# Performance work log

Hardware: AMD Instinct MI355X
Metric: run time of the kernel (lower is better)

## Reference

```python
import jax, jax.numpy as jnp
import numpy as np

T, B, I, H = 256, 32, 128, 256
CLIP = 2.0

def setup_inputs() -> dict:
    key = jax.random.key(0)
    ks = jax.random.split(key, 10)
    si, sh = 1.0 / np.sqrt(I), 1.0 / np.sqrt(H)
    return {
        "x":     jax.random.normal(ks[0], (T, B, I), jnp.float32),
        "Wx":    jax.random.normal(ks[1], (4 * H, I), jnp.float32) * si,
        "bx":    jax.random.normal(ks[2], (4 * H,), jnp.float32) * si,
        "Wh":    jax.random.normal(ks[3], (4 * H, H), jnp.float32) * sh,
        "bh":    jax.random.normal(ks[4], (4 * H,), jnp.float32) * sh,
        "w_mod": jax.random.normal(ks[5], (1, H), jnp.float32) * sh,
        "b_mod": jax.random.normal(ks[6], (1,), jnp.float32) * sh,
        "w_fan": jax.random.normal(ks[7], (H, 1), jnp.float32),
        "b_fan": jax.random.normal(ks[8], (H,), jnp.float32),
        "alpha": 1e-4 * jax.random.uniform(ks[9], (H, H), jnp.float32),
    }

def reference(x, Wx, bx, Wh, bh, w_mod, b_mod, w_fan, b_fan, alpha):
    Bn = x.shape[1]
    # precompute input projection for all timesteps: [T, B, 4H]
    xf = jnp.einsum('tbi,gi->tbg', x, Wx) + bx

    def step(state, xf_t):
        h, c, hebb = state  # h,c: [B,H]; hebb: [B,H,H]
        fioj = xf_t + h @ Wh.T + bh                     # [B,4H]
        f = jax.nn.sigmoid(fioj[:, :H])
        i = jax.nn.sigmoid(fioj[:, H:2 * H])
        o = jax.nn.sigmoid(fioj[:, 2 * H:3 * H])
        # h_pred @ (alpha * hebb) : batched vec-mat product
        plast = jnp.einsum('bh,hk,bhk->bk', h, alpha, hebb)
        j = jnp.tanh(fioj[:, 3 * H:] + plast)
        c_new = f * c + i * j
        h_new = o * jnp.tanh(c_new)
        eta = jnp.tanh(c_new @ w_mod.T + b_mod)          # [B,1]
        myeta = eta * w_fan[:, 0] + b_fan                # [B,H] (Linear(1,H) fanout)
        # delta_hebb = outer(h_pred, j); eta modulates along the j axis
        hebb_new = jnp.clip(hebb + myeta[:, None, :] * (h[:, :, None] * j[:, None, :]),
                            -CLIP, CLIP)
        return (h_new, c_new, hebb_new), h_new

    init = (jnp.zeros((Bn, H), jnp.float32),
            jnp.zeros((Bn, H), jnp.float32),
            jnp.zeros((Bn, H, H), jnp.float32))
    (h, c, hebb), hs = jax.lax.scan(step, init, xf)
    return hs, h, c, hebb
```

## Files before the change

kernel.cpp:

```cpp
#include <hip/hip_runtime.h>


#define TT 256
#define BB 32
#define II 128
#define HH 256
#define G4 1024

typedef _Float16 h2_t __attribute__((ext_vector_type(2)));
typedef unsigned long long u64;

__device__ __forceinline__ float sigm(float x) {
    return 1.0f / (1.0f + __expf(-x));
}
__device__ __forceinline__ float tanhfast(float x) {
    return 1.0f - 2.0f / (__expf(2.0f * x) + 1.0f);
}
__device__ __forceinline__ unsigned pkh(float lo, float hi) {
    h2_t v;
    v.x = (_Float16)lo;
    v.y = (_Float16)hi;
    return __builtin_bit_cast(unsigned, v);
}

#if __has_builtin(__builtin_amdgcn_fdot2)
__device__ __forceinline__ float dot2(unsigned a, unsigned b, float c) {
    return __builtin_amdgcn_fdot2(__builtin_bit_cast(h2_t, a),
                                  __builtin_bit_cast(h2_t, b), c, false);
}
#else
__device__ __forceinline__ float dot2(unsigned a, unsigned b, float c) {
    h2_t av = __builtin_bit_cast(h2_t, a), bv = __builtin_bit_cast(h2_t, b);
    return c + (float)av.x * (float)bv.x + (float)av.y * (float)bv.y;
}
#endif

__device__ __forceinline__ h2_t pkfma(h2_t a, h2_t b, h2_t c) {
#if __has_builtin(__builtin_elementwise_fma)
    return __builtin_elementwise_fma(a, b, c);
#else
    return a * b + c;
#endif
}
__device__ __forceinline__ h2_t clip2h(h2_t x) {
    const h2_t lo = {(_Float16)-2.0f, (_Float16)-2.0f};
    const h2_t hi = {(_Float16)2.0f, (_Float16)2.0f};
#if __has_builtin(__builtin_elementwise_max) && __has_builtin(__builtin_elementwise_min)
    return __builtin_elementwise_min(__builtin_elementwise_max(x, lo), hi);
#else
    h2_t r = x;
    r.x = r.x < lo.x ? lo.x : (r.x > hi.x ? hi.x : r.x);
    r.y = r.y < lo.y ? lo.y : (r.y > hi.y ? hi.y : r.y);
    return r;
#endif
}

__device__ __forceinline__ u64 spin_slot(const u64* fp, const u64* dp,
                                         unsigned tag) {
    u64 v;
    int it = 0;
    for (;;) {
        if ((it & 3) == 3) {
            v = __hip_atomic_load(dp, __ATOMIC_RELAXED,
                                  __HIP_MEMORY_SCOPE_AGENT);
        } else {
            asm volatile("global_load_dwordx2 %0, %1, off sc0\n\t"
                         "s_waitcnt vmcnt(0)"
                         : "=v"(v) : "v"(fp));
        }
        ++it;
        if ((unsigned)(v >> 32) == tag) return v;
    }
}

__global__ __launch_bounds__(256) void prep_wdx(const float* __restrict__ Wh,
                                                uint4* __restrict__ Wd) {
    int idx = blockIdx.x * 256 + threadIdx.x;
    int c = idx >> 10, g = idx & 1023;
    const float4* s = (const float4*)(Wh + (size_t)g * HH + (c << 3));
    float4 a = s[0], b2 = s[1];
    uint4 o;
    o.x = pkh(a.x, a.y);
    o.y = pkh(a.z, a.w);
    o.z = pkh(b2.x, b2.y);
    o.w = pkh(b2.z, b2.w);
    Wd[idx] = o;
}

__global__ __launch_bounds__(256) void prep_alq(const float* __restrict__ alpha,
                                                uint4* __restrict__ alQ) {
    int idx = blockIdx.x * 256 + threadIdx.x;
    int p4 = idx >> 8, k = idx & 255;
    unsigned r[4];
#pragma unroll
    for (int j = 0; j < 4; ++j) {
        int p = 4 * p4 + j;
        float a0 = alpha[(size_t)(2 * p) * HH + k];
        float a1 = alpha[(size_t)(2 * p + 1) * HH + k];
        r[j] = pkh(a0, a1);
    }
    uint4 o; o.x = r[0]; o.y = r[1]; o.z = r[2]; o.w = r[3];
    alQ[idx] = o;
}

__global__ __launch_bounds__(256) void xf_gemm(const float* __restrict__ x,
                                               const float* __restrict__ Wx,
                                               const float* __restrict__ bx,
                                               const float* __restrict__ bh,
                                               float* __restrict__ xf) {
    __shared__ float As[64][37];
    __shared__ float Bs[64][37];
    const int tid = threadIdx.x;
    const int tx = tid & 15, ty = tid >> 4;
    const int m0 = blockIdx.y << 6;
    const int n0 = blockIdx.x << 6;
    float c[4][4] = {};

    for (int k0 = 0; k0 < II; k0 += 32) {
#pragma unroll
        for (int hh = 0; hh < 2; ++hh) {
            int row = (tid >> 3) + (hh << 5);
            int col = (tid & 7) << 2;
            float4 va = *(const float4*)(x + (size_t)(m0 + row) * II + k0 + col);
            As[row][col] = va.x; As[row][col + 1] = va.y;
            As[row][col + 2] = va.z; As[row][col + 3] = va.w;
            float4 vb = *(const float4*)(Wx + (size_t)(n0 + row) * II + k0 + col);
            Bs[row][col] = vb.x; Bs[row][col + 1] = vb.y;
            Bs[row][col + 2] = vb.z; Bs[row][col + 3] = vb.w;
        }
        __syncthreads();
#pragma unroll
        for (int kk = 0; kk < 32; ++kk) {
            float a[4], bb[4];
#pragma unroll
            for (int u = 0; u < 4; ++u) a[u] = As[(ty << 2) + u][kk];
#pragma unroll
            for (int v = 0; v < 4; ++v) bb[v] = Bs[(tx << 2) + v][kk];
#pragma unroll
            for (int u = 0; u < 4; ++u)
#pragma unroll
                for (int v = 0; v < 4; ++v)
                    c[u][v] = fmaf(a[u], bb[v], c[u][v]);
        }
        __syncthreads();
    }
    const int n = n0 + (tx << 2);
    float4 bxv = *(const float4*)(bx + n);
    float4 bhv = *(const float4*)(bh + n);
    float4 badd = {bxv.x + bhv.x, bxv.y + bhv.y, bxv.z + bhv.z, bxv.w + bhv.w};
#pragma unroll
    for (int u = 0; u < 4; ++u) {
        int m = m0 + (ty << 2) + u;
        float4 o = {c[u][0] + badd.x, c[u][1] + badd.y,
                    c[u][2] + badd.z, c[u][3] + badd.w};
        *(float4*)(xf + (size_t)m * G4 + n) = o;
    }
}

#define HBQ_FOREACH(X) X(0) X(1) X(2) X(3) X(4) X(5) X(6) X(7)

#define HBQ_DECL(i) h2_t hp##i = {(_Float16)0.0f, (_Float16)0.0f};
#define HBQ_OUT(i) \
    hbout[(size_t)((rr << 4) + 2 * i) * HH + kcol]     = (float)hp##i.x; \
    hbout[(size_t)((rr << 4) + 2 * i + 1) * HH + kcol] = (float)hp##i.y;

#define HBQ_STEP(i, au, hou, hnu) { \
    h2_t al2 = __builtin_bit_cast(h2_t, au); \
    h2_t ho2 = __builtin_bit_cast(h2_t, hou); \
    h2_t hn2 = __builtin_bit_cast(h2_t, hnu); \
    hp##i = clip2h(pkfma(mj2, ho2, hp##i)); \
    h2_t hna = hn2 * al2; \
    pp = dot2(__builtin_bit_cast(unsigned, hna), \
              __builtin_bit_cast(unsigned, hp##i), pp); }

#define HBQ_CHUNK(q, AV, i0, i1, i2, i3) { \
    uint4 ho = hfO4[hb4 + (q)]; \
    uint4 hn = hfN4[hb4 + (q)]; \
    HBQ_STEP(i0, AV.x, ho.x, hn.x) \
    HBQ_STEP(i1, AV.y, ho.y, hn.y) \
    HBQ_STEP(i2, AV.z, ho.z, hn.z) \
    HBQ_STEP(i3, AV.w, ho.w, hn.w) }

#define HBV_STEP(i, hou) { \
    h2_t ho2 = __builtin_bit_cast(h2_t, hou); \
    hp##i = clip2h(pkfma(mj2, ho2, hp##i)); }
#define HBV_CHUNK(q, i0, i1, i2, i3) { \
    uint4 ho = hfO4[hb4 + (q)]; \
    HBV_STEP(i0, ho.x) HBV_STEP(i1, ho.y) \
    HBV_STEP(i2, ho.z) HBV_STEP(i3, ho.w) }

#define DOTW(W, HV) { \
    ac0 = dot2(W.x, HV.x, ac0); ac1 = dot2(W.y, HV.y, ac1); \
    ac2 = dot2(W.z, HV.z, ac2); ac3 = dot2(W.w, HV.w, ac3); }

#define PUB(slotoff, val32) { \
    u64 pkv = ((u64)tag << 32) | (u64)(val32); \
    __hip_atomic_store(&myF[slotoff], pkv, __ATOMIC_RELAXED, \
                       __HIP_MEMORY_SCOPE_WORKGROUP); \
    __hip_atomic_store(&myEx[slotoff], pkv, __ATOMIC_RELAXED, \
                       __HIP_MEMORY_SCOPE_AGENT); }

__global__ __launch_bounds__(1024, 1) void scan_kernel(
    const float* __restrict__ xf,
    const uint4* __restrict__ Wd,
    const uint4* __restrict__ alQ,
    const float* __restrict__ w_mod,
    const float* __restrict__ b_mod,
    const float* __restrict__ w_fan,
    const float* __restrict__ b_fan,
    u64* __restrict__ exData,
    u64* __restrict__ exFast,
    float* __restrict__ out) {
    const int bid = blockIdx.x;
    const int r   = bid >> 5;
    const int b   = bid & 31;
    const int tid = threadIdx.x;
    const int kk  = tid >> 8;
    const int m   = tid & 255;
    const int g   = ((m >> 6) << 8) + (r << 6) + (m & 63);
    const int rr  = tid >> 6;
    const int ch6 = tid & 63;
    const int kcol = (r << 6) + ch6;
    const int hb4 = rr << 1;

    __shared__ alignas(16) unsigned short hf_s[2][HH];
    __shared__ float part_s[G4];
    __shared__ float pp_s[G4];
    __shared__ alignas(16) float xfs[4][256];
    __shared__ float js[64];
    __shared__ float red_s[4];

    HBQ_FOREACH(HBQ_DECL)

    if (tid < HH) {
        hf_s[0][tid] = 0;
        hf_s[1][tid] = 0;
    }
    if (tid < 4) red_s[tid] = 0.0f;
    if (tid < 64) js[tid] = 0.0f;
    __syncthreads();

    const float bmod = b_mod[0];
    const float wfq = w_fan[kcol], bfq = b_fan[kcol];
    const float wmq = w_mod[kcol];
    float creg = 0.0f, hreg = 0.0f;

    const uint4* wb = Wd + ((size_t)(kk << 3) << 10) + g;
    uint4 w0 = wb[0],    w1 = wb[1024], w2 = wb[2048], w3 = wb[3072];
    uint4 w4 = wb[4096], w5 = wb[5120], w6 = wb[6144], w7 = wb[7168];
    uint4 aqA = alQ[(size_t)(hb4) * 256 + kcol];
    uint4 aqB = alQ[(size_t)(hb4 + 1) * 256 + kcol];

    u64* myEx = exData + ((size_t)(b * 4 + r) << 7);
    u64* myF  = exFast + ((size_t)(b * 4 + r) << 7);
    const int rp1 = (r + 1) & 3, rp2 = (r + 2) & 3, rp3 = (r + 3) & 3;
    const u64* pEx[3] = {exData + ((size_t)(b * 4 + rp1) << 7),
                         exData + ((size_t)(b * 4 + rp2) << 7),
                         exData + ((size_t)(b * 4 + rp3) << 7)};
    const u64* pF[3]  = {exFast + ((size_t)(b * 4 + rp1) << 7),
                         exFast + ((size_t)(b * 4 + rp2) << 7),
                         exFast + ((size_t)(b * 4 + rp3) << 7)};
    const int prole[3] = {rp1, rp2, rp3};

    for (int t = 0; t < TT; ++t) {
        const unsigned tag = (unsigned)(t + 1);
        const int sb = (t & 1) << 6;

        if ((t & 3) == 0) {
            const int d = tid >> 8;
            const int mm = tid & 255;
            const int gg = ((mm >> 6) << 8) + (r << 6) + (mm & 63);
            xfs[d][mm] = xf[(size_t)(t + d) * BB * G4 + (size_t)b * G4 + gg];
        }

        const uint4* hfO4 = (const uint4*)hf_s[t & 1];
        const uint4* hfN4 = (const uint4*)hf_s[(t & 1) ^ 1];

        float eta = tanhfast(((red_s[0] + red_s[1]) + (red_s[2] + red_s[3])) + bmod);
        float mj = fmaf(eta, wfq, bfq) * js[ch6];
        h2_t mj2;
        mj2.x = (_Float16)mj;
        mj2.y = mj2.x;
        float pp = 0.0f;
        HBQ_CHUNK(0, aqA, 0, 1, 2, 3)
        HBQ_CHUNK(1, aqB, 4, 5, 6, 7)
        pp_s[tid] = pp;

        float ac0 = 0.f, ac1 = 0.f, ac2 = 0.f, ac3 = 0.f;
        {
            const int hx = kk << 3;
            uint4 h0 = hfN4[hx], h1 = hfN4[hx + 1];
            uint4 h2 = hfN4[hx + 2], h3 = hfN4[hx + 3];
            DOTW(w0, h0) DOTW(w1, h1) DOTW(w2, h2) DOTW(w3, h3)
            uint4 h4 = hfN4[hx + 4], h5 = hfN4[hx + 5];
            uint4 h6 = hfN4[hx + 6], h7 = hfN4[hx + 7];
            DOTW(w4, h4) DOTW(w5, h5) DOTW(w6, h6) DOTW(w7, h7)
        }
        part_s[tid] = ((ac0 + ac1) + (ac2 + ac3));
        __syncthreads();

        if (tid < 64) {
            const int c6 = tid;
            float s0 = ((part_s[c6] + part_s[256 + c6]) +
                        (part_s[512 + c6] + part_s[768 + c6])) +
                       xfs[t & 3][c6];
            float s1 = ((part_s[64 + c6] + part_s[320 + c6]) +
                        (part_s[576 + c6] + part_s[832 + c6])) +
                       xfs[t & 3][64 + c6];
            float s2 = ((part_s[128 + c6] + part_s[384 + c6]) +
                        (part_s[640 + c6] + part_s[896 + c6])) +
                       xfs[t & 3][128 + c6];
            float s3 = ((part_s[192 + c6] + part_s[448 + c6]) +
                        (part_s[704 + c6] + part_s[960 + c6])) +
                       xfs[t & 3][192 + c6];
            float p01 = (pp_s[c6] + pp_s[64 + c6]) +
                        (pp_s[128 + c6] + pp_s[192 + c6]);
            float p23 = (pp_s[256 + c6] + pp_s[320 + c6]) +
                        (pp_s[384 + c6] + pp_s[448 + c6]);
            float p45 = (pp_s[512 + c6] + pp_s[576 + c6]) +
                        (pp_s[640 + c6] + pp_s[704 + c6]);
            float p67 = (pp_s[768 + c6] + pp_s[832 + c6]) +
                        (pp_s[896 + c6] + pp_s[960 + c6]);
            s3 += (p01 + p23) + (p45 + p67);

            float fg = sigm(s0);
            float ig = sigm(s1);
            float og = sigm(s2);
            float jv = tanhfast(s3);
            creg = fmaf(fg, creg, ig * jv);
            hreg = og * tanhfast(creg);
            js[c6] = jv;
            _Float16 hh = (_Float16)hreg;
            unsigned hu = (unsigned)__builtin_bit_cast(unsigned short, hh);
            hf_s[t & 1][(r << 6) + c6] = (unsigned short)hu;
            out[((size_t)t * BB + b) * HH + (r << 6) + c6] = hreg;

            float e = creg * wmq;
#pragma unroll
            for (int mm = 32; mm >= 1; mm >>= 1) e += __shfl_xor(e, mm, 64);

            unsigned other = (unsigned)__shfl_xor((int)hu, 1, 64);
            if ((c6 & 1) == 0) {
                unsigned pay = hu | (other << 16);
                PUB(sb + (c6 >> 1), pay)
            }
            if (c6 == 0) {
                red_s[r] = e;
                PUB(sb + 32, __builtin_bit_cast(unsigned, e))
            }
        }

        if (tid >= 64 && tid < 160) {
            const int p = (tid - 64) >> 5;
            const int s = (tid - 64) & 31;
            u64 v = spin_slot(pF[p] + sb + s, pEx[p] + sb + s, tag);
            ((unsigned*)hf_s[t & 1])[(prole[p] << 5) + s] = (unsigned)v;
        } else if (tid >= 160 && tid < 163) {
            const int p = tid - 160;
            u64 v = spin_slot(pF[p] + sb + 32, pEx[p] + sb + 32, tag);
            red_s[prole[p]] = __builtin_bit_cast(float, (unsigned)v);
        }
        __syncthreads();
    }

    {
        float eta = tanhfast(((red_s[0] + red_s[1]) + (red_s[2] + red_s[3])) + bmod);
        float mj = fmaf(eta, wfq, bfq) * js[ch6];
        h2_t mj2;
        mj2.x = (_Float16)mj;
        mj2.y = mj2.x;
        const uint4* hfO4 = (const uint4*)hf_s[0];
        HBV_CHUNK(0, 0, 1, 2, 3)
        HBV_CHUNK(1, 4, 5, 6, 7)
    }

    const size_t HS = (size_t)TT * BB * HH;
    if (tid < 64) {
        out[HS + (size_t)b * HH + kcol]           = hreg;
        out[HS + BB * HH + (size_t)b * HH + kcol] = creg;
    }
    float* hbout = out + HS + 2 * BB * HH + (size_t)b * HH * HH;
    HBQ_FOREACH(HBQ_OUT)
}

extern "C" void kernel_launch(void* const* d_in, const int* in_sizes, int n_in,
                              void* d_out, int out_size, void* d_ws,
                              size_t ws_size, hipStream_t stream) {
    const float* x     = (const float*)d_in[0];
    const float* Wx    = (const float*)d_in[1];
    const float* bx    = (const float*)d_in[2];
    const float* Wh    = (const float*)d_in[3];
    const float* bh    = (const float*)d_in[4];
    const float* w_mod = (const float*)d_in[5];
    const float* b_mod = (const float*)d_in[6];
    const float* w_fan = (const float*)d_in[7];
    const float* b_fan = (const float*)d_in[8];
    const float* alpha = (const float*)d_in[9];
    float* out = (float*)d_out;

    float* xf  = (float*)d_ws;
    uint4* Wd  = (uint4*)((char*)d_ws + 33554432);
    uint4* alQ = (uint4*)((char*)d_ws + 34078720);
    u64*   exD = (u64*)((char*)d_ws + 34209792);
    u64*   exF = (u64*)((char*)d_ws + 34340864);

    hipLaunchKernelGGL(prep_wdx, dim3(128), dim3(256), 0, stream, Wh, Wd);
    hipLaunchKernelGGL(prep_alq, dim3(32), dim3(256), 0, stream, alpha, alQ);
    hipLaunchKernelGGL(xf_gemm, dim3(16, 128), dim3(256), 0, stream,
                       x, Wx, bx, bh, xf);
    hipLaunchKernelGGL(scan_kernel, dim3(128), dim3(1024), 0, stream,
                       xf, Wd, alQ, w_mod, b_mod, w_fan, b_fan,
                       exD, exF, out);
}
```

Baseline: 796.5 us.

## Remap thread roles so partial sums reduce via wave shuffles instead of LDS

Reassigns threads so the K-split partials of each gate output and the 16 hebb row-group partials per column sit in adjacent lanes of one wavefront. Both are then reduced with xor shuffles, and only one lane writes to small shared arrays. This removes the 1024-entry part_s/pp_s buffers and the 32-load serial reduction the 64 gate threads did on the critical path of each step. It also moves the h publish ahead of the local stores and the eta reduction, to shorten the latency between steps. The cost is more shuffle work spread across all threads, and a changed hebb output store pattern that may coalesce worse.

```diff
diff --git a/kernel.cpp b/kernel.cpp
--- a/kernel.cpp
+++ b/kernel.cpp
@@ -161,8 +161,8 @@
 
 #define HBQ_DECL(i) h2_t hp##i = {(_Float16)0.0f, (_Float16)0.0f};
 #define HBQ_OUT(i) \
-    hbout[(size_t)((rr << 4) + 2 * i) * HH + kcol]     = (float)hp##i.x; \
-    hbout[(size_t)((rr << 4) + 2 * i + 1) * HH + kcol] = (float)hp##i.y;
+    hbout[(size_t)((rg16 << 4) + 2 * i) * HH + kcolh]     = (float)hp##i.x; \
+    hbout[(size_t)((rg16 << 4) + 2 * i + 1) * HH + kcolh] = (float)hp##i.y;
 
 #define HBQ_STEP(i, au, hou, hnu) { \
     h2_t al2 = __builtin_bit_cast(h2_t, au); \
@@ -173,9 +173,9 @@
     pp = dot2(__builtin_bit_cast(unsigned, hna), \
               __builtin_bit_cast(unsigned, hp##i), pp); }
 
-#define HBQ_CHUNK(q, AV, i0, i1, i2, i3) { \
-    uint4 ho = hfO4[hb4 + (q)]; \
-    uint4 hn = hfN4[hb4 + (q)]; \
+#define HBQ_CHUNK(cq, AV, i0, i1, i2, i3) { \
+    uint4 ho = hfO4[hb4 + (cq)]; \
+    uint4 hn = hfN4[hb4 + (cq)]; \
     HBQ_STEP(i0, AV.x, ho.x, hn.x) \
     HBQ_STEP(i1, AV.y, ho.y, hn.y) \
     HBQ_STEP(i2, AV.z, ho.z, hn.z) \
@@ -184,8 +184,8 @@
 #define HBV_STEP(i, hou) { \
     h2_t ho2 = __builtin_bit_cast(h2_t, hou); \
     hp##i = clip2h(pkfma(mj2, ho2, hp##i)); }
-#define HBV_CHUNK(q, i0, i1, i2, i3) { \
-    uint4 ho = hfO4[hb4 + (q)]; \
+#define HBV_CHUNK(cq, i0, i1, i2, i3) { \
+    uint4 ho = hfO4[hb4 + (cq)]; \
     HBV_STEP(i0, ho.x) HBV_STEP(i1, ho.y) \
     HBV_STEP(i2, ho.z) HBV_STEP(i3, ho.w) }
 
@@ -215,17 +215,17 @@
     const int r   = bid >> 5;
     const int b   = bid & 31;
     const int tid = threadIdx.x;
-    const int kk  = tid >> 8;
-    const int m   = tid & 255;
-    const int g   = ((m >> 6) << 8) + (r << 6) + (m & 63);
-    const int rr  = tid >> 6;
-    const int ch6 = tid & 63;
-    const int kcol = (r << 6) + ch6;
-    const int hb4 = rr << 1;
+    const int c6h  = tid >> 4;
+    const int rg16 = tid & 15;
+    const int kcolh = (r << 6) + c6h;
+    const int hb4   = rg16 << 1;
+    const int q    = tid & 3;
+    const int gidx = tid >> 2;
+    const int g    = ((gidx >> 6) << 8) + (r << 6) + (gidx & 63);
 
     __shared__ alignas(16) unsigned short hf_s[2][HH];
-    __shared__ float part_s[G4];
-    __shared__ float pp_s[G4];
+    __shared__ float gate_s[256];
+    __shared__ float ppsum_s[64];
     __shared__ alignas(16) float xfs[4][256];
     __shared__ float js[64];
     __shared__ float red_s[4];
@@ -241,15 +241,15 @@
     __syncthreads();
 
     const float bmod = b_mod[0];
-    const float wfq = w_fan[kcol], bfq = b_fan[kcol];
-    const float wmq = w_mod[kcol];
+    const float wfq = w_fan[kcolh], bfq = b_fan[kcolh];
+    const float wm2 = w_mod[(r << 6) + (tid & 63)];
     float creg = 0.0f, hreg = 0.0f;
 
-    const uint4* wb = Wd + ((size_t)(kk << 3) << 10) + g;
+    const uint4* wb = Wd + ((size_t)(q << 3) << 10) + g;
     uint4 w0 = wb[0],    w1 = wb[1024], w2 = wb[2048], w3 = wb[3072];
     uint4 w4 = wb[4096], w5 = wb[5120], w6 = wb[6144], w7 = wb[7168];
-    uint4 aqA = alQ[(size_t)(hb4) * 256 + kcol];
-    uint4 aqB = alQ[(size_t)(hb4 + 1) * 256 + kcol];
+    uint4 aqA = alQ[(size_t)(hb4) * 256 + kcolh];
+    uint4 aqB = alQ[(size_t)(hb4 + 1) * 256 + kcolh];
 
     u64* myEx = exData + ((size_t)(b * 4 + r) << 7);
     u64* myF  = exFast + ((size_t)(b * 4 + r) << 7);
@@ -277,18 +277,22 @@
         const uint4* hfN4 = (const uint4*)hf_s[(t & 1) ^ 1];
 
         float eta = tanhfast(((red_s[0] + red_s[1]) + (red_s[2] + red_s[3])) + bmod);
-        float mj = fmaf(eta, wfq, bfq) * js[ch6];
+        float mj = fmaf(eta, wfq, bfq) * js[c6h];
         h2_t mj2;
         mj2.x = (_Float16)mj;
         mj2.y = mj2.x;
         float pp = 0.0f;
         HBQ_CHUNK(0, aqA, 0, 1, 2, 3)
         HBQ_CHUNK(1, aqB, 4, 5, 6, 7)
-        pp_s[tid] = pp;
+        pp += __shfl_xor(pp, 1, 64);
+        pp += __shfl_xor(pp, 2, 64);
+        pp += __shfl_xor(pp, 4, 64);
+        pp += __shfl_xor(pp, 8, 64);
+        if (rg16 == 0) ppsum_s[c6h] = pp;
 
         float ac0 = 0.f, ac1 = 0.f, ac2 = 0.f, ac3 = 0.f;
         {
-            const int hx = kk << 3;
+            const int hx = q << 3;
             uint4 h0 = hfN4[hx], h1 = hfN4[hx + 1];
             uint4 h2 = hfN4[hx + 2], h3 = hfN4[hx + 3];
             DOTW(w0, h0) DOTW(w1, h1) DOTW(w2, h2) DOTW(w3, h3)
@@ -296,54 +300,38 @@
             uint4 h6 = hfN4[hx + 6], h7 = hfN4[hx + 7];
             DOTW(w4, h4) DOTW(w5, h5) DOTW(w6, h6) DOTW(w7, h7)
         }
-        part_s[tid] = ((ac0 + ac1) + (ac2 + ac3));
+        float ac = (ac0 + ac1) + (ac2 + ac3);
+        ac += __shfl_xor(ac, 1, 64);
+        ac += __shfl_xor(ac, 2, 64);
+        if (q == 0) gate_s[gidx] = ac;
         __syncthreads();
 
         if (tid < 64) {
             const int c6 = tid;
-            float s0 = ((part_s[c6] + part_s[256 + c6]) +
-                        (part_s[512 + c6] + part_s[768 + c6])) +
-                       xfs[t & 3][c6];
-            float s1 = ((part_s[64 + c6] + part_s[320 + c6]) +
-                        (part_s[576 + c6] + part_s[832 + c6])) +
-                       xfs[t & 3][64 + c6];
-            float s2 = ((part_s[128 + c6] + part_s[384 + c6]) +
-                        (part_s[640 + c6] + part_s[896 + c6])) +
-                       xfs[t & 3][128 + c6];
-            float s3 = ((part_s[192 + c6] + part_s[448 + c6]) +
-                        (part_s[704 + c6] + part_s[960 + c6])) +
-                       xfs[t & 3][192 + c6];
-            float p01 = (pp_s[c6] + pp_s[64 + c6]) +
-                        (pp_s[128 + c6] + pp_s[192 + c6]);
-            float p23 = (pp_s[256 + c6] + pp_s[320 + c6]) +
-                        (pp_s[384 + c6] + pp_s[448 + c6]);
-            float p45 = (pp_s[512 + c6] + pp_s[576 + c6]) +
-                        (pp_s[640 + c6] + pp_s[704 + c6]);
-            float p67 = (pp_s[768 + c6] + pp_s[832 + c6]) +
-                        (pp_s[896 + c6] + pp_s[960 + c6]);
-            s3 += (p01 + p23) + (p45 + p67);
-
+            const float* xr = xfs[t & 3];
+            float s0 = gate_s[c6] + xr[c6];
+            float s1 = gate_s[64 + c6] + xr[64 + c6];
+            float s2 = gate_s[128 + c6] + xr[128 + c6];
+            float s3 = (gate_s[192 + c6] + xr[192 + c6]) + ppsum_s[c6];
             float fg = sigm(s0);
             float ig = sigm(s1);
             float og = sigm(s2);
             float jv = tanhfast(s3);
             creg = fmaf(fg, creg, ig * jv);
             hreg = og * tanhfast(creg);
-            js[c6] = jv;
             _Float16 hh = (_Float16)hreg;
             unsigned hu = (unsigned)__builtin_bit_cast(unsigned short, hh);
-            hf_s[t & 1][(r << 6) + c6] = (unsigned short)hu;
-            out[((size_t)t * BB + b) * HH + (r << 6) + c6] = hreg;
-
-            float e = creg * wmq;
-#pragma unroll
-            for (int mm = 32; mm >= 1; mm >>= 1) e += __shfl_xor(e, mm, 64);
-
             unsigned other = (unsigned)__shfl_xor((int)hu, 1, 64);
             if ((c6 & 1) == 0) {
                 unsigned pay = hu | (other << 16);
                 PUB(sb + (c6 >> 1), pay)
             }
+            js[c6] = jv;
+            hf_s[t & 1][(r << 6) + c6] = (unsigned short)hu;
+            out[((size_t)t * BB + b) * HH + (r << 6) + c6] = hreg;
+            float e = creg * wm2;
+#pragma unroll
+            for (int mm = 32; mm >= 1; mm >>= 1) e += __shfl_xor(e, mm, 64);
             if (c6 == 0) {
                 red_s[r] = e;
                 PUB(sb + 32, __builtin_bit_cast(unsigned, e))
@@ -365,7 +353,7 @@
 
     {
         float eta = tanhfast(((red_s[0] + red_s[1]) + (red_s[2] + red_s[3])) + bmod);
-        float mj = fmaf(eta, wfq, bfq) * js[ch6];
+        float mj = fmaf(eta, wfq, bfq) * js[c6h];
         h2_t mj2;
         mj2.x = (_Float16)mj;
         mj2.y = mj2.x;
@@ -376,8 +364,8 @@
 
     const size_t HS = (size_t)TT * BB * HH;
     if (tid < 64) {
-        out[HS + (size_t)b * HH + kcol]           = hreg;
-        out[HS + BB * HH + (size_t)b * HH + kcol] = creg;
+        out[HS + (size_t)b * HH + (r << 6) + tid]           = hreg;
+        out[HS + BB * HH + (size_t)b * HH + (r << 6) + tid] = creg;
     }
     float* hbout = out + HS + 2 * BB * HH + (size_t)b * HH * HH;
     HBQ_FOREACH(HBQ_OUT)
```

New measurement: 870.3 us. 1.09x slower.
